# Kernel tuning notes

Measured on AMD Instinct MI355X. Metric: run time of the kernel, lower is better.

Reference implementation:

```python
import jax, jax.numpy as jnp
import numpy as np

B, T, N = 64, 500, 2048
THRESHOLD = 1.0
BETA_RES = 0.9      # beta_reservoir
BETA_IN = 0.8       # input_lif_beta
SPECTRAL_RADIUS = 0.9
INIT_A, INIT_B = -1.0, 1.0


def setup_inputs() -> dict:
    key = jax.random.key(0)
    k1, k2, k3 = jax.random.split(key, 3)
    x = jax.random.normal(k1, (B, T, 1), dtype=jnp.float32)
    w_in = jax.random.normal(k2, (1, 1), dtype=jnp.float32)      # input_fc weight (out=1, in=1)
    w_res_in = jax.random.normal(k3, (N, 1), dtype=jnp.float32)  # reservoir_fc weight (out=N, in=1)
    # Recurrent weights: uniform[a,b] then rescale to desired spectral radius (done in numpy, matches init-time torch code)
    rng = np.random.default_rng(0)
    W = rng.uniform(INIT_A, INIT_B, size=(N, N)).astype(np.float32)
    radius = np.abs(np.linalg.eigvals(W)).max()
    W = W * (SPECTRAL_RADIUS / radius)
    W_rec = jnp.asarray(W, dtype=jnp.float32)
    return {"x": x, "w_in": w_in, "w_res_in": w_res_in, "W_rec": W_rec}


def reference(x, w_in, w_res_in, W_rec):
    """Vmem input path: input LIF integrates without spiking; reservoir is an
    all-to-all recurrent LIF with zero reset. Returns (avg_firing_rate, spike_record, mem_record)."""
    dtype = x.dtype
    imem0 = jnp.zeros((x.shape[0], 1), dtype)
    mem0 = jnp.zeros((x.shape[0], N), dtype)
    spk0 = jnp.zeros((x.shape[0], N), dtype)

    def step(carry, x_t):
        imem, mem, spk = carry
        # input LIF membrane (no spike/reset in 'Vmem' mode)
        imem = BETA_IN * imem + x_t @ w_in.T                      # (B,1)
        cur = imem @ w_res_in.T                                   # (B,N)
        # reservoir RLeaky, zero reset based on previous spikes, recurrent all-to-all
        mem = BETA_RES * mem * (1.0 - spk) + cur + spk @ W_rec.T  # (B,N)
        spk = (mem > THRESHOLD).astype(dtype)
        return (imem, mem, spk), (spk, mem)

    xs = jnp.transpose(x, (1, 0, 2))  # (T,B,1)
    _, (spike_record, mem_record) = jax.lax.scan(step, (imem0, mem0, spk0), xs)
    avg_firing_rate = spike_record.mean()
    return avg_firing_rate, spike_record, mem_record
```

## Files before the change

### kernel.cpp

```cpp
#include <hip/hip_runtime.h>

typedef int v4i __attribute__((ext_vector_type(4)));

#define WMAX_OFF   0
#define CNT_OFF    4
#define EP_OFF     8
#define IMEM_OFF   64
#define PK_OFF     131072
#define FLAGS_OFF  196608
#define WFRAG_OFF  262144

__global__ void sr_prep(const float* __restrict__ x, const float* __restrict__ w_in,
                        float* __restrict__ imem, unsigned* wmax_bits, unsigned* cnt,
                        unsigned* ep) {
  int b = threadIdx.x;
  if (b == 64) *wmax_bits = 0u;
  if (b == 65) *cnt = 0u;
  if (b == 66) *ep += 1024u;
  if (b < 64) {
    float wi = w_in[0];
    float im = 0.0f;
    for (int t0 = 0; t0 < 500; t0 += 10) {
      float xs[10];
      #pragma unroll
      for (int j = 0; j < 10; ++j) xs[j] = x[b * 500 + t0 + j];
      #pragma unroll
      for (int j = 0; j < 10; ++j) {
        im = 0.8f * im + xs[j] * wi;
        imem[(t0 + j) * 64 + b] = im;
      }
    }
  }
}

__global__ void sr_wmax(const float* __restrict__ W, unsigned* wmax_bits) {
  __shared__ unsigned sm;
  if (threadIdx.x == 0) sm = 0u;
  __syncthreads();
  float m = 0.0f;
  for (size_t i = (size_t)blockIdx.x * 256 + threadIdx.x; i < 4194304ull; i += 262144ull)
    m = fmaxf(m, fabsf(W[i]));
  atomicMax(&sm, __float_as_uint(m));
  __syncthreads();
  if (threadIdx.x == 0) atomicMax(wmax_bits, sm);
}

__global__ void sr_wquant(const float* __restrict__ W, const unsigned* __restrict__ wmax_bits,
                          v4i* __restrict__ wfr) {
  __shared__ float ws[16][257];
  const int p = blockIdx.x >> 3;
  const int w = blockIdx.x & 7;
  const int tid = threadIdx.x;
  {
    int r = tid >> 5;
    int c0 = (tid & 31) * 8;
    const float* src = W + (size_t)(p * 16 + r) * 2048 + 256 * w + c0;
    #pragma unroll
    for (int j = 0; j < 8; ++j) ws[r][c0 + j] = src[j];
  }
  __syncthreads();
  const int fl = tid >> 6;
  const int kl = fl >> 1, sp = fl & 1;
  const int lane = tid & 63;
  const int col = lane & 15;
  const int q = lane >> 4;
  const float S = 32000.0f / __uint_as_float(*wmax_bits);
  int dw[4] = {0, 0, 0, 0};
  #pragma unroll
  for (int j = 0; j < 16; ++j) {
    int d = j >> 2, i = j & 3;
    float wv = ws[col][(4 * kl + q) * 16 + 4 * i + d];
    int qv = (int)rintf(wv * S);
    int hi = (qv + 128) >> 8;
    int lo = qv - (hi << 8);
    int v = sp ? lo : hi;
    dw[d] |= (v & 255) << (8 * i);
  }
  v4i o; o[0] = dw[0]; o[1] = dw[1]; o[2] = dw[2]; o[3] = dw[3];
  wfr[(size_t)((((p * 8 + w) * 4 + kl) * 2 + sp)) * 64 + lane] = o;
}

__global__ __launch_bounds__(512, 2)
void sr_main(const float* __restrict__ imem, const v4i* __restrict__ wfr,
             unsigned* pk, unsigned* flags, const unsigned* __restrict__ ep,
             const float* __restrict__ w_res, const unsigned* __restrict__ wmax_bits,
             unsigned* cnt_g, float* __restrict__ out) {
  extern __shared__ char smem_raw[];
  v4i* redv = (v4i*)smem_raw;
  int* outl = (int*)(smem_raw + 32768);

  const int p = blockIdx.x;
  const int tid = threadIdx.x;
  const int w = tid >> 6;
  const int lane = tid & 63;
  const int q = lane >> 4;
  const int col = lane & 15;
  const unsigned base = *ep;

  v4i wf[4][2];
  #pragma unroll
  for (int kl = 0; kl < 4; ++kl)
    #pragma unroll
    for (int sp = 0; sp < 2; ++sp)
      wf[kl][sp] = wfr[(size_t)((((p * 8 + w) * 4 + kl) * 2 + sp)) * 64 + lane];

  const int be = tid >> 3;
  const int h = tid & 7;
  const int nl = h * 2;
  const float wr0 = w_res[p * 16 + nl + 0];
  const float wr1 = w_res[p * 16 + nl + 1];
  float mem0 = 0, mem1 = 0, sp0 = 0, sp1 = 0;
  int cnt = 0;
  const float invS = __uint_as_float(*wmax_bits) / 32000.0f;
  const v4i vzero = {0, 0, 0, 0};
  const int pubshift = (h >> 1) * 8 + 2 * (h & 1) + 4 * (be & 1);
  const int sh2 = (col & 1) * 4;
  const int cc = col >> 1;

  for (int t = 0; t < 500; ++t) {
    float im = imem[t * 64 + be];
    float rec0 = 0, rec1 = 0;
    if (t > 0) {
      const unsigned tgt = base + (unsigned)t;
      {
        const unsigned* fp = flags + (size_t)(t & 1) * 128 + 16 * w + (lane & 15);
        unsigned fv = __hip_atomic_load(fp, __ATOMIC_RELAXED, __HIP_MEMORY_SCOPE_AGENT);
        int guard = 0;
        while (!__all(fv == tgt)) {
          __builtin_amdgcn_s_sleep(1);
          fv = __hip_atomic_load(fp, __ATOMIC_RELAXED, __HIP_MEMORY_SCOPE_AGENT);
          if (++guard > (1 << 20)) break;
        }
      }

      unsigned ww[16];
      {
        const unsigned* srcb = pk + (size_t)((t - 1) & 1) * 4096 + (16 * w + q) * 32 + cc;
        #pragma unroll
        for (int f = 0; f < 16; ++f) {
          int kl = f & 3, bt = f >> 2;
          ww[f] = __hip_atomic_load(srcb + kl * 128 + bt * 8,
                                    __ATOMIC_RELAXED, __HIP_MEMORY_SCOPE_AGENT);
        }
      }

      v4i acc[4][2];
      #pragma unroll
      for (int bt = 0; bt < 4; ++bt) { acc[bt][0] = vzero; acc[bt][1] = vzero; }
      #pragma unroll
      for (int f = 0; f < 16; ++f) {
        int kl = f & 3, bt = f >> 2;
        unsigned wbs = ww[f] >> sh2;
        v4i a;
        a[0] = (int)((wbs >> 0) & 0x01010101u);
        a[1] = (int)((wbs >> 1) & 0x01010101u);
        a[2] = (int)((wbs >> 2) & 0x01010101u);
        a[3] = (int)((wbs >> 3) & 0x01010101u);
        acc[bt][0] = __builtin_amdgcn_mfma_i32_16x16x64_i8(a, wf[kl][0], acc[bt][0], 0, 0, 0);
        acc[bt][1] = __builtin_amdgcn_mfma_i32_16x16x64_i8(a, wf[kl][1], acc[bt][1], 0, 0, 0);
      }
      #pragma unroll
      for (int bt = 0; bt < 4; ++bt) {
        v4i c = acc[bt][0] * 256 + acc[bt][1];
        redv[(w * 4 + bt) * 64 + lane] = c;
      }
      __syncthreads();
      if (w < 4) {
        v4i s = vzero;
        #pragma unroll
        for (int ww2 = 0; ww2 < 8; ++ww2) s += redv[(ww2 * 4 + w) * 64 + lane];
        int ob = (w * 16 + (lane >> 4) * 4) * 16 + (lane & 15);
        outl[ob]      = s[0];
        outl[ob + 16] = s[1];
        outl[ob + 32] = s[2];
        outl[ob + 48] = s[3];
      }
      __syncthreads();
      int2 rv = *(const int2*)(outl + be * 16 + nl);
      rec0 = (float)rv.x * invS;
      rec1 = (float)rv.y * invS;
    }

    mem0 = 0.9f * mem0 * (1.0f - sp0) + im * wr0 + rec0;
    mem1 = 0.9f * mem1 * (1.0f - sp1) + im * wr1 + rec1;
    int s0i = mem0 > 1.0f, s1i = mem1 > 1.0f;
    sp0 = (float)s0i; sp1 = (float)s1i;

    unsigned v = ((unsigned)(s0i | (s1i << 1))) << pubshift;
    v |= (unsigned)__shfl_xor((int)v, 1);
    v |= (unsigned)__shfl_xor((int)v, 2);
    v |= (unsigned)__shfl_xor((int)v, 4);
    v |= (unsigned)__shfl_xor((int)v, 8);
    if ((tid & 15) == 0)
      __hip_atomic_store(&pk[(size_t)(t & 1) * 4096 + p * 32 + (tid >> 4)], v,
                         __ATOMIC_RELAXED, __HIP_MEMORY_SCOPE_AGENT);
    __syncthreads();
    if (tid == 0)
      __hip_atomic_store(&flags[(size_t)((t + 1) & 1) * 128 + p], base + (unsigned)(t + 1),
                         __ATOMIC_RELAXED, __HIP_MEMORY_SCOPE_AGENT);
    cnt += s0i + s1i;

    size_t sb = 1ull + (size_t)t * 131072ull + (size_t)be * 2048ull + (size_t)(p * 16 + nl);
    __builtin_nontemporal_store(sp0, out + sb + 0);
    __builtin_nontemporal_store(sp1, out + sb + 1);
    __builtin_nontemporal_store(mem0, out + sb + 65536000ull + 0);
    __builtin_nontemporal_store(mem1, out + sb + 65536000ull + 1);
  }

  __syncthreads();
  int* csh = (int*)smem_raw;
  if (tid == 0) csh[0] = 0;
  __syncthreads();
  atomicAdd(csh, cnt);
  __syncthreads();
  if (tid == 0) atomicAdd(cnt_g, (unsigned)csh[0]);
}

__global__ void sr_fin(const unsigned* __restrict__ cnt, float* __restrict__ out) {
  out[0] = (float)((double)(*cnt) / 65536000.0);
}

extern "C" void kernel_launch(void* const* d_in, const int* in_sizes, int n_in,
                              void* d_out, int out_size, void* d_ws, size_t ws_size,
                              hipStream_t stream) {
  const float* x     = (const float*)d_in[0];
  const float* w_in  = (const float*)d_in[1];
  const float* w_res = (const float*)d_in[2];
  const float* W     = (const float*)d_in[3];
  float* out = (float*)d_out;
  char* ws = (char*)d_ws;

  unsigned* wmax_bits = (unsigned*)(ws + WMAX_OFF);
  unsigned* cntp      = (unsigned*)(ws + CNT_OFF);
  unsigned* ep        = (unsigned*)(ws + EP_OFF);
  float* imem         = (float*)(ws + IMEM_OFF);
  unsigned* pkt       = (unsigned*)(ws + PK_OFF);
  unsigned* flg       = (unsigned*)(ws + FLAGS_OFF);
  v4i* wfr            = (v4i*)(ws + WFRAG_OFF);

  sr_prep<<<1, 128, 0, stream>>>(x, w_in, imem, wmax_bits, cntp, ep);
  sr_wmax<<<1024, 256, 0, stream>>>(W, wmax_bits);
  sr_wquant<<<1024, 512, 0, stream>>>(W, wmax_bits, wfr);
  sr_main<<<128, 512, 36864, stream>>>(imem, wfr, pkt, flg, ep, w_res, wmax_bits, cntp, out);
  sr_fin<<<1, 1, 0, stream>>>(cntp, out);
}
```

Baseline: 2.254 ms.

## Split batch into two halves pipelined across grid with per-wave flags and LDS-staged spikes

Splits each timestep into two batch-half phases, each with its own spike buffers and per-wave readiness flags. Blocks can then start the matmul for one half while other blocks are still publishing the other half. Spike words are loaded cooperatively into LDS once per phase instead of each wave issuing redundant global atomic loads. Flags are now published per wave after a vmcnt wait instead of after a block barrier. The cost is more barriers per step, finer-grained flag polling, and a flag array that grows to 1024 entries per parity.

```diff
diff --git a/kernel.cpp b/kernel.cpp
--- a/kernel.cpp
+++ b/kernel.cpp
@@ -1,6 +1,7 @@
 #include <hip/hip_runtime.h>
 
 typedef int v4i __attribute__((ext_vector_type(4)));
+typedef unsigned u32x4 __attribute__((ext_vector_type(4)));
 
 #define WMAX_OFF   0
 #define CNT_OFF    4
@@ -86,8 +87,9 @@
              const float* __restrict__ w_res, const unsigned* __restrict__ wmax_bits,
              unsigned* cnt_g, float* __restrict__ out) {
   extern __shared__ char smem_raw[];
-  v4i* redv = (v4i*)smem_raw;
-  int* outl = (int*)(smem_raw + 32768);
+  unsigned* spk_lds = (unsigned*)smem_raw;
+  v4i* redv = (v4i*)(smem_raw + 8192);
+  int* outl = (int*)(smem_raw + 24576);
 
   const int p = blockIdx.x;
   const int tid = threadIdx.x;
@@ -116,95 +118,104 @@
   const int pubshift = (h >> 1) * 8 + 2 * (h & 1) + 4 * (be & 1);
   const int sh2 = (col & 1) * 4;
   const int cc = col >> 1;
+  const int mygroup = w >> 2;
 
   for (int t = 0; t < 500; ++t) {
     float im = imem[t * 64 + be];
-    float rec0 = 0, rec1 = 0;
-    if (t > 0) {
-      const unsigned tgt = base + (unsigned)t;
-      {
-        const unsigned* fp = flags + (size_t)(t & 1) * 128 + 16 * w + (lane & 15);
+    #pragma unroll
+    for (int g = 0; g < 2; ++g) {
+      float rec0 = 0, rec1 = 0;
+      if (t > 0) {
+        const unsigned tgt = base + (unsigned)t;
+        const unsigned* fp = flags + (size_t)(t & 1) * 1024 + (tid >> 2) * 8 + 4 * g + (tid & 3);
         unsigned fv = __hip_atomic_load(fp, __ATOMIC_RELAXED, __HIP_MEMORY_SCOPE_AGENT);
         int guard = 0;
-        while (!__all(fv == tgt)) {
+        while (fv != tgt && ++guard < (1 << 20)) {
           __builtin_amdgcn_s_sleep(1);
           fv = __hip_atomic_load(fp, __ATOMIC_RELAXED, __HIP_MEMORY_SCOPE_AGENT);
-          if (++guard > (1 << 20)) break;
-        }
-      }
-
-      unsigned ww[16];
-      {
-        const unsigned* srcb = pk + (size_t)((t - 1) & 1) * 4096 + (16 * w + q) * 32 + cc;
-        #pragma unroll
-        for (int f = 0; f < 16; ++f) {
-          int kl = f & 3, bt = f >> 2;
-          ww[f] = __hip_atomic_load(srcb + kl * 128 + bt * 8,
-                                    __ATOMIC_RELAXED, __HIP_MEMORY_SCOPE_AGENT);
-        }
-      }
-
-      v4i acc[4][2];
-      #pragma unroll
-      for (int bt = 0; bt < 4; ++bt) { acc[bt][0] = vzero; acc[bt][1] = vzero; }
-      #pragma unroll
-      for (int f = 0; f < 16; ++f) {
-        int kl = f & 3, bt = f >> 2;
-        unsigned wbs = ww[f] >> sh2;
-        v4i a;
-        a[0] = (int)((wbs >> 0) & 0x01010101u);
-        a[1] = (int)((wbs >> 1) & 0x01010101u);
-        a[2] = (int)((wbs >> 2) & 0x01010101u);
-        a[3] = (int)((wbs >> 3) & 0x01010101u);
-        acc[bt][0] = __builtin_amdgcn_mfma_i32_16x16x64_i8(a, wf[kl][0], acc[bt][0], 0, 0, 0);
-        acc[bt][1] = __builtin_amdgcn_mfma_i32_16x16x64_i8(a, wf[kl][1], acc[bt][1], 0, 0, 0);
-      }
-      #pragma unroll
-      for (int bt = 0; bt < 4; ++bt) {
-        v4i c = acc[bt][0] * 256 + acc[bt][1];
-        redv[(w * 4 + bt) * 64 + lane] = c;
+        }
+        const unsigned* src = pk + (size_t)((t - 1) & 1) * 4096 + g * 2048 + tid * 4;
+        unsigned q0 = __hip_atomic_load(src + 0, __ATOMIC_RELAXED, __HIP_MEMORY_SCOPE_AGENT);
+        unsigned q1 = __hip_atomic_load(src + 1, __ATOMIC_RELAXED, __HIP_MEMORY_SCOPE_AGENT);
+        unsigned q2 = __hip_atomic_load(src + 2, __ATOMIC_RELAXED, __HIP_MEMORY_SCOPE_AGENT);
+        unsigned q3 = __hip_atomic_load(src + 3, __ATOMIC_RELAXED, __HIP_MEMORY_SCOPE_AGENT);
+        u32x4 qv = {q0, q1, q2, q3};
+        *(u32x4*)(spk_lds + tid * 4) = qv;
       }
       __syncthreads();
-      if (w < 4) {
+
+      if (t > 0) {
+        unsigned ww[8];
+        #pragma unroll
+        for (int f = 0; f < 8; ++f) {
+          int kl = f & 3, bt2 = f >> 2;
+          ww[f] = spk_lds[(16 * w + 4 * kl + q) * 16 + bt2 * 8 + cc];
+        }
+        v4i acc[2][2];
+        acc[0][0] = vzero; acc[0][1] = vzero; acc[1][0] = vzero; acc[1][1] = vzero;
+        #pragma unroll
+        for (int f = 0; f < 8; ++f) {
+          int kl = f & 3, bt2 = f >> 2;
+          unsigned wbs = ww[f] >> sh2;
+          v4i a;
+          a[0] = (int)((wbs >> 0) & 0x01010101u);
+          a[1] = (int)((wbs >> 1) & 0x01010101u);
+          a[2] = (int)((wbs >> 2) & 0x01010101u);
+          a[3] = (int)((wbs >> 3) & 0x01010101u);
+          acc[bt2][0] = __builtin_amdgcn_mfma_i32_16x16x64_i8(a, wf[kl][0], acc[bt2][0], 0, 0, 0);
+          acc[bt2][1] = __builtin_amdgcn_mfma_i32_16x16x64_i8(a, wf[kl][1], acc[bt2][1], 0, 0, 0);
+        }
+        #pragma unroll
+        for (int bt2 = 0; bt2 < 2; ++bt2) {
+          v4i c = acc[bt2][0] * 256 + acc[bt2][1];
+          redv[(w * 2 + bt2) * 64 + lane] = c;
+        }
+      }
+      __syncthreads();
+      if (t > 0 && w < 2) {
         v4i s = vzero;
         #pragma unroll
-        for (int ww2 = 0; ww2 < 8; ++ww2) s += redv[(ww2 * 4 + w) * 64 + lane];
-        int ob = (w * 16 + (lane >> 4) * 4) * 16 + (lane & 15);
+        for (int k = 0; k < 8; ++k) s += redv[(k * 2 + w) * 64 + lane];
+        int ob = (w * 16 + (lane >> 4) * 4) * 16 + col;
         outl[ob]      = s[0];
         outl[ob + 16] = s[1];
         outl[ob + 32] = s[2];
         outl[ob + 48] = s[3];
       }
       __syncthreads();
-      int2 rv = *(const int2*)(outl + be * 16 + nl);
-      rec0 = (float)rv.x * invS;
-      rec1 = (float)rv.y * invS;
+
+      if (mygroup == g) {
+        if (t > 0) {
+          int2 rv = *(const int2*)(outl + (be & 31) * 16 + nl);
+          rec0 = (float)rv.x * invS;
+          rec1 = (float)rv.y * invS;
+        }
+        mem0 = 0.9f * mem0 * (1.0f - sp0) + im * wr0 + rec0;
+        mem1 = 0.9f * mem1 * (1.0f - sp1) + im * wr1 + rec1;
+        int s0i = mem0 > 1.0f, s1i = mem1 > 1.0f;
+        sp0 = (float)s0i; sp1 = (float)s1i;
+
+        unsigned v = ((unsigned)(s0i | (s1i << 1))) << pubshift;
+        v |= (unsigned)__shfl_xor((int)v, 1);
+        v |= (unsigned)__shfl_xor((int)v, 2);
+        v |= (unsigned)__shfl_xor((int)v, 4);
+        v |= (unsigned)__shfl_xor((int)v, 8);
+        if ((tid & 15) == 0)
+          __hip_atomic_store(pk + (size_t)(t & 1) * 4096 + g * 2048 + p * 16 + (w & 3) * 4 + (lane >> 4),
+                             v, __ATOMIC_RELAXED, __HIP_MEMORY_SCOPE_AGENT);
+        asm volatile("s_waitcnt vmcnt(0)" ::: "memory");
+        if (lane == 0)
+          __hip_atomic_store(flags + (size_t)((t + 1) & 1) * 1024 + p * 8 + w,
+                             base + (unsigned)(t + 1), __ATOMIC_RELAXED, __HIP_MEMORY_SCOPE_AGENT);
+        cnt += s0i + s1i;
+
+        size_t sb = 1ull + (size_t)t * 131072ull + (size_t)be * 2048ull + (size_t)(p * 16 + nl);
+        __builtin_nontemporal_store(sp0, out + sb + 0);
+        __builtin_nontemporal_store(sp1, out + sb + 1);
+        __builtin_nontemporal_store(mem0, out + sb + 65536000ull + 0);
+        __builtin_nontemporal_store(mem1, out + sb + 65536000ull + 1);
+      }
     }
-
-    mem0 = 0.9f * mem0 * (1.0f - sp0) + im * wr0 + rec0;
-    mem1 = 0.9f * mem1 * (1.0f - sp1) + im * wr1 + rec1;
-    int s0i = mem0 > 1.0f, s1i = mem1 > 1.0f;
-    sp0 = (float)s0i; sp1 = (float)s1i;
-
-    unsigned v = ((unsigned)(s0i | (s1i << 1))) << pubshift;
-    v |= (unsigned)__shfl_xor((int)v, 1);
-    v |= (unsigned)__shfl_xor((int)v, 2);
-    v |= (unsigned)__shfl_xor((int)v, 4);
-    v |= (unsigned)__shfl_xor((int)v, 8);
-    if ((tid & 15) == 0)
-      __hip_atomic_store(&pk[(size_t)(t & 1) * 4096 + p * 32 + (tid >> 4)], v,
-                         __ATOMIC_RELAXED, __HIP_MEMORY_SCOPE_AGENT);
-    __syncthreads();
-    if (tid == 0)
-      __hip_atomic_store(&flags[(size_t)((t + 1) & 1) * 128 + p], base + (unsigned)(t + 1),
-                         __ATOMIC_RELAXED, __HIP_MEMORY_SCOPE_AGENT);
-    cnt += s0i + s1i;
-
-    size_t sb = 1ull + (size_t)t * 131072ull + (size_t)be * 2048ull + (size_t)(p * 16 + nl);
-    __builtin_nontemporal_store(sp0, out + sb + 0);
-    __builtin_nontemporal_store(sp1, out + sb + 1);
-    __builtin_nontemporal_store(mem0, out + sb + 65536000ull + 0);
-    __builtin_nontemporal_store(mem1, out + sb + 65536000ull + 1);
   }
 
   __syncthreads();
@@ -241,6 +252,6 @@
   sr_prep<<<1, 128, 0, stream>>>(x, w_in, imem, wmax_bits, cntp, ep);
   sr_wmax<<<1024, 256, 0, stream>>>(W, wmax_bits);
   sr_wquant<<<1024, 512, 0, stream>>>(W, wmax_bits, wfr);
-  sr_main<<<128, 512, 36864, stream>>>(imem, wfr, pkt, flg, ep, w_res, wmax_bits, cntp, out);
+  sr_main<<<128, 512, 26624, stream>>>(imem, wfr, pkt, flg, ep, w_res, wmax_bits, cntp, out);
   sr_fin<<<1, 1, 0, stream>>>(cntp, out);
 }
```

Result: slower. 3.420 ms (+51.7%).
